# Optimization experiments

Hardware: AMD Instinct MI355X
Metric: run time of the kernel (lower is better)

Reference implementation:

```python
import jax, jax.numpy as jnp
import numpy as np

SPS_AMPLIFY = 1.5
SPS_DAMPEN = 0.3
SPS_DEEP_QUESTION = 0.1
SPS_EXCLAIM = 0.85
SPS_QUESTION = 0.25
SPS_SUPER_EXCLAIM = 0.95

B, S, D = 4, 2048, 1024
NUM_HEADS = 16
HEAD_DIM = D // NUM_HEADS
SCALE = HEAD_DIM ** (-0.5)


def sps_pro(x):
    """Piecewise elementwise modulation based on sigmoid(x) bands."""
    xn = jax.nn.sigmoid(x)
    # bands: xn>0.95 -> 2.0 ; 0.85<xn<=0.95 -> 1.5 ; xn<0.1 -> 0.1 ;
    #        0.1<=xn<0.25 -> 0.3 ; else -> 1.0
    mult = jnp.where(
        xn > SPS_SUPER_EXCLAIM, 2.0,
        jnp.where(xn > SPS_EXCLAIM, SPS_AMPLIFY,
                  jnp.where(xn < SPS_DEEP_QUESTION, 0.1,
                            jnp.where(xn < SPS_QUESTION, SPS_DAMPEN, 1.0))))
    return x * mult


def setup_inputs() -> dict:
    key = jax.random.key(0)
    k0, k1, k2, k3, k4 = jax.random.split(key, 5)
    s = 1.0 / np.sqrt(D)
    return {
        "x": jax.random.normal(k0, (B, S, D), dtype=jnp.float32),
        "W_qkv": jax.random.uniform(k1, (D, 3 * D), dtype=jnp.float32, minval=-s, maxval=s),
        "b_qkv": jax.random.uniform(k2, (3 * D,), dtype=jnp.float32, minval=-s, maxval=s),
        "W_proj": jax.random.uniform(k3, (D, D), dtype=jnp.float32, minval=-s, maxval=s),
        "b_proj": jax.random.uniform(k4, (D,), dtype=jnp.float32, minval=-s, maxval=s),
    }


def reference(x, W_qkv, b_qkv, W_proj, b_proj):
    qkv = jnp.einsum('bsd,de->bse', x, W_qkv) + b_qkv  # [B,S,3D]
    q, k, v = jnp.split(qkv, 3, axis=-1)               # each [B,S,D]
    attn = jnp.einsum('bsd,btd->bst', q, k) * SCALE    # [B,S,S]
    attn = sps_pro(attn)
    attn = jax.nn.softmax(attn, axis=-1)
    out = jnp.einsum('bst,btd->bsd', attn, v)          # [B,S,D]
    out = jnp.einsum('bsd,de->bse', out, W_proj) + b_proj
    return out
```

## Files before the change

### kernel.cpp

```cpp
#include <hip/hip_runtime.h>
#include <hip/hip_bf16.h>
#include <hip/hip_fp16.h>
#include <stdint.h>

typedef __attribute__((ext_vector_type(8))) _Float16 f16x8;
typedef __attribute__((ext_vector_type(4))) float f32x4;

__device__ __forceinline__ void async16(void* lds, const void* g) {
  __builtin_amdgcn_global_load_lds(
      (const __attribute__((address_space(1))) void*)g,
      (__attribute__((address_space(3))) void*)lds, 16, 0, 0);
}

__device__ __forceinline__ uint16_t f2h_u(float f) {
  union { __half h; uint16_t u; } c;
  c.h = __float2half(f);
  return c.u;
}

__global__ __launch_bounds__(256)
void conv_f2h(const float* __restrict__ in, uint16_t* __restrict__ out, int n4) {
  int i = blockIdx.x * 256 + threadIdx.x;
  if (i >= n4) return;
  float4 v = ((const float4*)in)[i];
  ushort4 o;
  o.x = f2h_u(v.x); o.y = f2h_u(v.y); o.z = f2h_u(v.z); o.w = f2h_u(v.w);
  ((ushort4*)out)[i] = o;
}

__global__ __launch_bounds__(256)
void trans_f2h(const float* __restrict__ in, uint16_t* __restrict__ out,
               int ldin, int ldout) {
  __shared__ float t[64][65];
  const int tx = threadIdx.x & 63, ty = threadIdx.x >> 6;
  const int r0 = blockIdx.y * 64, c0 = blockIdx.x * 64;
#pragma unroll
  for (int i = 0; i < 16; ++i)
    t[ty + i * 4][tx] = in[(size_t)(r0 + ty + i * 4) * ldin + c0 + tx];
  __syncthreads();
#pragma unroll
  for (int i = 0; i < 16; ++i)
    out[(size_t)(c0 + ty + i * 4) * ldout + r0 + tx] = f2h_u(t[tx][ty + i * 4]);
}

template <int EPI>
__global__ __launch_bounds__(512, 2)
void gemm8p(const uint16_t* __restrict__ A, const uint16_t* __restrict__ B,
            void* __restrict__ Cv, void* __restrict__ Cv2, void* __restrict__ Cv3,
            const float* __restrict__ bias,
            int nT, int lda, int ldb, int ldc,
            long long strA, long long strB, long long strC) {
  extern __shared__ uint16_t lds_u16[];

  const int gx = gridDim.x, gy = gridDim.y;
  const int nwg = gx * gy * gridDim.z;
  const int fid = blockIdx.x + gx * (blockIdx.y + gy * blockIdx.z);
  const int fs = (fid & 7) * (nwg >> 3) + (fid >> 3);
  const int bx = fs % gx;
  const int by = (fs / gx) % gy;
  const int bz = fs / (gx * gy);

  const int tid = threadIdx.x;
  const int l = tid & 63;
  const int w = tid >> 6;
  const int wm = w >> 2, wn = w & 3;
  const int l15 = l & 15, l4 = l >> 4;
  const int rowBase = bx * 256, colBase = by * 256;
  const uint16_t* Ag = A + (size_t)bz * strA;
  const uint16_t* Bg = B + (size_t)bz * strB;

  const uint16_t* sA[2][2];
  const uint16_t* sB[2][2];
#pragma unroll
  for (int u = 0; u < 2; ++u) {
    int c = tid + (u << 9);
    int cs = c ^ ((c >> 3) & 7);
    int row = cs >> 3, kc = (cs & 7) * 8;
    sA[0][u] = Ag + (size_t)(rowBase + row) * lda + kc;
    sA[1][u] = Ag + (size_t)(rowBase + 128 + row) * lda + kc;
    sB[0][u] = Bg + (size_t)(colBase + row) * ldb + kc;
    sB[1][u] = Bg + (size_t)(colBase + 128 + row) * ldb + kc;
  }

  f32x4 acc[8][4];
#pragma unroll
  for (int m = 0; m < 8; ++m)
#pragma unroll
    for (int n = 0; n < 4; ++n)
      acc[m][n] = (f32x4){0.f, 0.f, 0.f, 0.f};

#define SH_A(buf, h, koff)                                                     \
  {                                                                            \
    const uint32_t d_ = (buf)*32768u + (h)*8192u;                              \
    async16(&lds_u16[d_ + (size_t)tid * 8], sA[h][0] + (koff));                \
    async16(&lds_u16[d_ + (size_t)(tid + 512) * 8], sA[h][1] + (koff));        \
  }
#define SH_B(buf, h, koff)                                                     \
  {                                                                            \
    const uint32_t d_ = (buf)*32768u + 16384u + (h)*8192u;                     \
    async16(&lds_u16[d_ + (size_t)tid * 8], sB[h][0] + (koff));                \
    async16(&lds_u16[d_ + (size_t)(tid + 512) * 8], sB[h][1] + (koff));        \
  }
#define RD_A(dst, buf, mh)                                                     \
  _Pragma("unroll") for (int mr = 0; mr < 4; ++mr) {                           \
    const int lr = (mh)*64 + mr * 16 + l15;                                    \
    const char* hb = (const char*)lds_u16 + (buf)*65536 + wm * 16384;          \
    _Pragma("unroll") for (int ks = 0; ks < 2; ++ks)                           \
      dst[mr][ks] = *(const f16x8*)(hb + lr * 128 +                            \
                    ((ks * 64 + l4 * 16) ^ ((lr & 7) << 4)));                  \
  }
#define RD_B(dst, buf, nh)                                                     \
  _Pragma("unroll") for (int nr = 0; nr < 2; ++nr) {                           \
    const int lr = (wn & 1) * 64 + (nh)*32 + nr * 16 + l15;                    \
    const char* hb = (const char*)lds_u16 + (buf)*65536 + 32768 +              \
                     (wn >> 1) * 16384;                                        \
    _Pragma("unroll") for (int ks = 0; ks < 2; ++ks)                           \
      dst[nr][ks] = *(const f16x8*)(hb + lr * 128 +                            \
                    ((ks * 64 + l4 * 16) ^ ((lr & 7) << 4)));                  \
  }
#define MM(m0, n0, AF, BF)                                                     \
  __builtin_amdgcn_s_setprio(1);                                               \
  _Pragma("unroll") for (int ks = 0; ks < 2; ++ks)                             \
  _Pragma("unroll") for (int mr = 0; mr < 4; ++mr)                             \
  _Pragma("unroll") for (int nr = 0; nr < 2; ++nr)                             \
    acc[(m0) + mr][(n0) + nr] = __builtin_amdgcn_mfma_f32_16x16x32_f16(        \
        AF[mr][ks], BF[nr][ks], acc[(m0) + mr][(n0) + nr], 0, 0, 0);           \
  __builtin_amdgcn_s_setprio(0);
#define VMC(n) asm volatile("s_waitcnt vmcnt(" #n ")" ::: "memory");
#define BAR() __builtin_amdgcn_s_barrier();

  SH_A(0, 0, 0) SH_A(0, 1, 0) SH_B(0, 0, 0) SH_B(0, 1, 0)
  SH_B(1, 0, 64) SH_B(1, 1, 64)
  VMC(4)
  BAR()

  const int nIter = nT >> 1;
  for (int i = 0; i < nIter; ++i) {
    const int e2 = 2 * i + 2, o = 2 * i + 1, o2 = 2 * i + 3;
    const int ke2 = e2 << 6, ko = o << 6, ko2 = o2 << 6;
    f16x8 a0[4][2], a1[4][2], b0[2][2], b1[2][2];
    RD_A(a0, 0, 0) RD_B(b0, 0, 0)
    SH_A(1, 0, ko)
    BAR()
    MM(0, 0, a0, b0)
    RD_B(b1, 0, 1)
    SH_A(1, 1, ko)
    BAR()
    MM(0, 2, a0, b1)
    RD_A(a1, 0, 1)
    if (e2 < nT) SH_B(0, 0, ke2)
    BAR()
    MM(4, 2, a1, b1)
    if (e2 < nT) { SH_B(0, 1, ke2) VMC(4) } else { VMC(0) }
    BAR()
    MM(4, 0, a1, b0)
    RD_A(a0, 1, 0) RD_B(b0, 1, 0)
    if (e2 < nT) SH_A(0, 0, ke2)
    BAR()
    MM(0, 0, a0, b0)
    RD_B(b1, 1, 1)
    if (e2 < nT) SH_A(0, 1, ke2)
    BAR()
    MM(0, 2, a0, b1)
    RD_A(a1, 1, 1)
    if (o2 < nT) SH_B(1, 0, ko2)
    BAR()
    MM(4, 2, a1, b1)
    if (o2 < nT) { SH_B(1, 1, ko2) }
    if (i + 1 < nIter) { if (o2 < nT) { VMC(4) } else { VMC(0) } }
    BAR()
    MM(4, 0, a1, b0)
  }
#undef SH_A
#undef SH_B
#undef RD_A
#undef RD_B
#undef MM
#undef VMC
#undef BAR

  if (EPI == 0) {
    uint16_t* qd = (uint16_t*)Cv;
    uint16_t* kd = (uint16_t*)Cv2;
    uint16_t* vt = (uint16_t*)Cv3;
#pragma unroll
    for (int ni = 0; ni < 4; ++ni) {
      const int gcol = colBase + wn * 64 + ni * 16 + l15;
      const float bv = bias[gcol];
      if (gcol < 2048) {
        uint16_t* base = (gcol < 1024 ? qd : kd) + (gcol & 1023);
#pragma unroll
        for (int mi = 0; mi < 8; ++mi)
#pragma unroll
          for (int j = 0; j < 4; ++j) {
            const int grow = rowBase + wm * 128 + mi * 16 + l4 * 4 + j;
            base[(size_t)(grow >> 11) * 2097152 + (size_t)(grow & 2047) * 1024] =
                f2h_u(acc[mi][ni][j] + bv);
          }
      } else {
        const int d = gcol - 2048;
#pragma unroll
        for (int mi = 0; mi < 8; ++mi) {
          const int grow0 = rowBase + wm * 128 + mi * 16 + l4 * 4;
          ushort4 o;
          o.x = f2h_u(acc[mi][ni][0] + bv);
          o.y = f2h_u(acc[mi][ni][1] + bv);
          o.z = f2h_u(acc[mi][ni][2] + bv);
          o.w = f2h_u(acc[mi][ni][3] + bv);
          *(ushort4*)&vt[(size_t)(grow0 >> 11) * 2097152 + (size_t)d * 2048 +
                         (grow0 & 2047)] = o;
        }
      }
    }
  } else {
    uint16_t* C = (uint16_t*)Cv + (size_t)bz * strC;
#pragma unroll
    for (int ni = 0; ni < 4; ++ni) {
      const int gcol = colBase + wn * 64 + ni * 16 + l15;
#pragma unroll
      for (int mi = 0; mi < 8; ++mi)
#pragma unroll
        for (int j = 0; j < 4; ++j) {
          const int grow = rowBase + wm * 128 + mi * 16 + l4 * 4 + j;
          float xs = acc[mi][ni][j] * 0.125f;
          float mult = (xs > 2.94443897916644f) ? 2.0f
                     : (xs > 1.73460105538811f) ? 1.5f
                     : (xs < -2.19722457733622f) ? 0.1f
                     : (xs < -1.09861228866811f) ? 0.3f
                                                 : 1.0f;
          C[(size_t)grow * ldc + gcol] = f2h_u(xs * mult);
        }
    }
  }
}

template <int EPI>
__global__ __launch_bounds__(512, 2)
void gemm_sm(const uint16_t* __restrict__ A, const uint16_t* __restrict__ B,
             void* __restrict__ Cv, const float* __restrict__ bias,
             int nT, int lda, int ldb, int ldc,
             long long strA, long long strB, long long strC) {
  extern __shared__ uint16_t lds_u16[];

  const int gx = gridDim.x, gy = gridDim.y;
  const int nwg = gx * gy * gridDim.z;
  const int fid = blockIdx.x + gx * (blockIdx.y + gy * blockIdx.z);
  const int fs = (fid & 7) * (nwg >> 3) + (fid >> 3);
  const int bx = fs % gx;
  const int by = (fs / gx) % gy;
  const int bz = fs / (gx * gy);

  const int tid = threadIdx.x;
  const int l = tid & 63;
  const int w = tid >> 6;
  const int wm = w >> 1, wn = w & 1;
  const int l15 = l & 15, l4 = l >> 4;
  const int rowBase = bx * 256, colBase = by * 128;
  const uint16_t* Ag = A + (size_t)bz * strA;
  const uint16_t* Bg = B + (size_t)bz * strB;

  const uint16_t* pA[4];
  const uint16_t* pB[2];
#pragma unroll
  for (int u = 0; u < 4; ++u) {
    int c = tid + (u << 9);
    int cs = c ^ ((c >> 3) & 7);
    pA[u] = Ag + (size_t)(rowBase + (cs >> 3)) * lda + (cs & 7) * 8;
  }
#pragma unroll
  for (int u = 0; u < 2; ++u) {
    int c = tid + (u << 9);
    int cs = c ^ ((c >> 3) & 7);
    pB[u] = Bg + (size_t)(colBase + (cs >> 3)) * ldb + (cs & 7) * 8;
  }

  f32x4 acc[4][4];
#pragma unroll
  for (int m = 0; m < 4; ++m)
#pragma unroll
    for (int n = 0; n < 4; ++n)
      acc[m][n] = (f32x4){0.f, 0.f, 0.f, 0.f};

#define STAGE(t2, s2)                                                          \
  {                                                                            \
    const int kb_ = (t2) << 6;                                                 \
    uint16_t* dA_ = lds_u16 + (s2) * 24576;                                    \
    uint16_t* dB_ = dA_ + 16384;                                               \
    _Pragma("unroll") for (int u = 0; u < 4; ++u)                              \
        async16(&dA_[(size_t)(tid + (u << 9)) * 8], pA[u] + kb_);              \
    _Pragma("unroll") for (int u = 0; u < 2; ++u)                              \
        async16(&dB_[(size_t)(tid + (u << 9)) * 8], pB[u] + kb_);              \
  }

  STAGE(0, 0)
  STAGE(1, 1)
  asm volatile("s_waitcnt vmcnt(6)" ::: "memory");
  __builtin_amdgcn_s_barrier();

  int sl = 0;
  for (int t = 0; t < nT; ++t) {
    int s2 = sl + 2; if (s2 >= 3) s2 -= 3;
    if (t + 2 < nT) STAGE(t + 2, s2)
    const uint16_t* As = lds_u16 + sl * 24576;
    const uint16_t* Bs = As + 16384;
#pragma unroll
    for (int ks = 0; ks < 2; ++ks) {
      f16x8 af[4], bf[4];
#pragma unroll
      for (int m = 0; m < 4; ++m) {
        const int r = wm * 64 + m * 16 + l15;
        const int byt = r * 128 + ((ks * 64 + l4 * 16) ^ ((r & 7) << 4));
        af[m] = *(const f16x8*)((const char*)As + byt);
      }
#pragma unroll
      for (int n = 0; n < 4; ++n) {
        const int r = wn * 64 + n * 16 + l15;
        const int byt = r * 128 + ((ks * 64 + l4 * 16) ^ ((r & 7) << 4));
        bf[n] = *(const f16x8*)((const char*)Bs + byt);
      }
      __builtin_amdgcn_s_setprio(1);
#pragma unroll
      for (int m = 0; m < 4; ++m)
#pragma unroll
        for (int n = 0; n < 4; ++n)
          acc[m][n] = __builtin_amdgcn_mfma_f32_16x16x32_f16(af[m], bf[n], acc[m][n], 0, 0, 0);
      __builtin_amdgcn_s_setprio(0);
    }
    if (t + 1 < nT) {
      if (t + 2 < nT) {
        asm volatile("s_waitcnt vmcnt(6)" ::: "memory");
      } else {
        asm volatile("s_waitcnt vmcnt(0)" ::: "memory");
      }
      __builtin_amdgcn_s_barrier();
    }
    sl = (sl == 2) ? 0 : sl + 1;
  }
#undef STAGE

  const int orow0 = rowBase + wm * 64 + l4 * 4;
  const int ocol0 = colBase + wn * 64 + l15;
  if (EPI == 3) {
    uint16_t* C = (uint16_t*)Cv + (size_t)bz * strC;
#pragma unroll
    for (int n = 0; n < 4; ++n)
#pragma unroll
      for (int m = 0; m < 4; ++m)
#pragma unroll
        for (int j = 0; j < 4; ++j)
          C[(size_t)(orow0 + m * 16 + j) * ldc + ocol0 + n * 16] = f2h_u(acc[m][n][j]);
  } else {
    float* C = (float*)Cv;
#pragma unroll
    for (int n = 0; n < 4; ++n) {
      const float bv = bias[ocol0 + n * 16];
#pragma unroll
      for (int m = 0; m < 4; ++m)
#pragma unroll
        for (int j = 0; j < 4; ++j)
          C[(size_t)(orow0 + m * 16 + j) * ldc + ocol0 + n * 16] = acc[m][n][j] + bv;
    }
  }
}

__global__ __launch_bounds__(256)
void softmax_rows(uint16_t* __restrict__ P) {
  const size_t row = blockIdx.x;
  uint16_t* p = P + row * 2048;
  const int tid = threadIdx.x;
  uint4 raw = *(const uint4*)(p + tid * 8);
  uint32_t w[4] = {raw.x, raw.y, raw.z, raw.w};
  float v[8];
#pragma unroll
  for (int q = 0; q < 4; ++q) {
    __half2 h = *(__half2*)&w[q];
    float2 f = __half22float2(h);
    v[2 * q] = f.x;
    v[2 * q + 1] = f.y;
  }
  float mx = v[0];
#pragma unroll
  for (int j = 1; j < 8; ++j) mx = fmaxf(mx, v[j]);
#pragma unroll
  for (int o = 32; o > 0; o >>= 1) mx = fmaxf(mx, __shfl_xor(mx, o));
  __shared__ float redm[4], reds[4];
  if ((tid & 63) == 0) redm[tid >> 6] = mx;
  __syncthreads();
  mx = fmaxf(fmaxf(redm[0], redm[1]), fmaxf(redm[2], redm[3]));
  float e[8];
  float se = 0.f;
#pragma unroll
  for (int j = 0; j < 8; ++j) { e[j] = __expf(v[j] - mx); se += e[j]; }
#pragma unroll
  for (int o = 32; o > 0; o >>= 1) se += __shfl_xor(se, o);
  if ((tid & 63) == 0) reds[tid >> 6] = se;
  __syncthreads();
  se = (reds[0] + reds[1]) + (reds[2] + reds[3]);
  const float inv = 1.0f / se;
  uint32_t wo[4];
#pragma unroll
  for (int q = 0; q < 4; ++q) {
    uint16_t a = f2h_u(e[2 * q] * inv);
    uint16_t b = f2h_u(e[2 * q + 1] * inv);
    wo[q] = (uint32_t)a | ((uint32_t)b << 16);
  }
  uint4 ov;
  ov.x = wo[0]; ov.y = wo[1]; ov.z = wo[2]; ov.w = wo[3];
  *(uint4*)(p + tid * 8) = ov;
}

extern "C" void kernel_launch(void* const* d_in, const int* in_sizes, int n_in,
                              void* d_out, int out_size, void* d_ws, size_t ws_size,
                              hipStream_t stream) {
  const float* x     = (const float*)d_in[0];
  const float* Wqkv  = (const float*)d_in[1];
  const float* bqkv  = (const float*)d_in[2];
  const float* Wproj = (const float*)d_in[3];
  const float* bproj = (const float*)d_in[4];
  float* out = (float*)d_out;

  char* ws = (char*)d_ws;
  size_t off = 0;
  auto alloc = [&](size_t bytes) -> void* {
    void* p = ws + off;
    off += (bytes + 255) & ~(size_t)255;
    return p;
  };
  uint16_t* xh    = (uint16_t*)alloc(8192ULL * 1024 * 2);
  uint16_t* WqkvT = (uint16_t*)alloc(3072ULL * 1024 * 2);
  uint16_t* WpT   = (uint16_t*)alloc(1024ULL * 1024 * 2);
  uint16_t* qh    = (uint16_t*)alloc(4ULL * 2048 * 1024 * 2);
  uint16_t* kh    = (uint16_t*)alloc(4ULL * 2048 * 1024 * 2);
  uint16_t* vT    = (uint16_t*)alloc(4ULL * 1024 * 2048 * 2);
  uint16_t* Pm    = (uint16_t*)alloc(4ULL * 2048 * 2048 * 2);
  uint16_t* ao    = xh;

  conv_f2h<<<8192, 256, 0, stream>>>(x, xh, 2097152);
  trans_f2h<<<dim3(48, 16), 256, 0, stream>>>(Wqkv, WqkvT, 3072, 1024);
  trans_f2h<<<dim3(16, 16), 256, 0, stream>>>(Wproj, WpT, 1024, 1024);
  gemm8p<0><<<dim3(32, 12, 1), 512, 131072, stream>>>(
      xh, WqkvT, qh, kh, vT, bqkv, 16, 1024, 1024, 0, 0, 0, 0);
  gemm8p<1><<<dim3(8, 8, 4), 512, 131072, stream>>>(
      qh, kh, Pm, nullptr, nullptr, nullptr, 16, 1024, 1024, 2048,
      2097152LL, 2097152LL, 4194304LL);
  softmax_rows<<<8192, 256, 0, stream>>>(Pm);
  gemm_sm<3><<<dim3(8, 8, 4), 512, 147456, stream>>>(
      Pm, vT, ao, nullptr, 32, 2048, 2048, 1024,
      4194304LL, 2097152LL, 2097152LL);
  gemm_sm<4><<<dim3(32, 8, 1), 512, 147456, stream>>>(
      ao, WpT, out, bproj, 16, 1024, 1024, 1024, 0, 0, 0);
}
```

Baseline: 214.7 us.

## Use smaller 128x128 double-buffered GEMM tiles for attention and projection

Replaces the 256x128 triple-buffered 512-thread GEMM with a 128x128 tile, 256-thread, double-buffered variant using 64KB LDS. The QK^T GEMM moves from the large gemm8p kernel onto this new kernel, with the sps modulation epilogue folded into it. The intent is more workgroups, lower LDS use and better occupancy and wave balance across CUs. The cost is less data reuse per tile and a shallower prefetch pipeline, since each step now waits for vmcnt(0).

Measured after the change: 214.8 us. Within noise of the previous version (+0.0%).

```diff
diff --git a/kernel.cpp b/kernel.cpp
--- a/kernel.cpp
+++ b/kernel.cpp
@@ -212,31 +212,12 @@
         }
       }
     }
-  } else {
-    uint16_t* C = (uint16_t*)Cv + (size_t)bz * strC;
-#pragma unroll
-    for (int ni = 0; ni < 4; ++ni) {
-      const int gcol = colBase + wn * 64 + ni * 16 + l15;
-#pragma unroll
-      for (int mi = 0; mi < 8; ++mi)
-#pragma unroll
-        for (int j = 0; j < 4; ++j) {
-          const int grow = rowBase + wm * 128 + mi * 16 + l4 * 4 + j;
-          float xs = acc[mi][ni][j] * 0.125f;
-          float mult = (xs > 2.94443897916644f) ? 2.0f
-                     : (xs > 1.73460105538811f) ? 1.5f
-                     : (xs < -2.19722457733622f) ? 0.1f
-                     : (xs < -1.09861228866811f) ? 0.3f
-                                                 : 1.0f;
-          C[(size_t)grow * ldc + gcol] = f2h_u(xs * mult);
-        }
-    }
   }
 }
 
 template <int EPI>
-__global__ __launch_bounds__(512, 2)
-void gemm_sm(const uint16_t* __restrict__ A, const uint16_t* __restrict__ B,
+__global__ __launch_bounds__(256, 2)
+void gemm_mb(const uint16_t* __restrict__ A, const uint16_t* __restrict__ B,
              void* __restrict__ Cv, const float* __restrict__ bias,
              int nT, int lda, int ldb, int ldc,
              long long strA, long long strB, long long strC) {
@@ -255,22 +236,17 @@
   const int w = tid >> 6;
   const int wm = w >> 1, wn = w & 1;
   const int l15 = l & 15, l4 = l >> 4;
-  const int rowBase = bx * 256, colBase = by * 128;
+  const int rowBase = bx * 128, colBase = by * 128;
   const uint16_t* Ag = A + (size_t)bz * strA;
   const uint16_t* Bg = B + (size_t)bz * strB;
 
   const uint16_t* pA[4];
-  const uint16_t* pB[2];
+  const uint16_t* pB[4];
 #pragma unroll
   for (int u = 0; u < 4; ++u) {
-    int c = tid + (u << 9);
+    int c = tid + (u << 8);
     int cs = c ^ ((c >> 3) & 7);
     pA[u] = Ag + (size_t)(rowBase + (cs >> 3)) * lda + (cs & 7) * 8;
-  }
-#pragma unroll
-  for (int u = 0; u < 2; ++u) {
-    int c = tid + (u << 9);
-    int cs = c ^ ((c >> 3) & 7);
     pB[u] = Bg + (size_t)(colBase + (cs >> 3)) * ldb + (cs & 7) * 8;
   }
 
@@ -284,25 +260,23 @@
 #define STAGE(t2, s2)                                                          \
   {                                                                            \
     const int kb_ = (t2) << 6;                                                 \
-    uint16_t* dA_ = lds_u16 + (s2) * 24576;                                    \
-    uint16_t* dB_ = dA_ + 16384;                                               \
-    _Pragma("unroll") for (int u = 0; u < 4; ++u)                              \
-        async16(&dA_[(size_t)(tid + (u << 9)) * 8], pA[u] + kb_);              \
-    _Pragma("unroll") for (int u = 0; u < 2; ++u)                              \
-        async16(&dB_[(size_t)(tid + (u << 9)) * 8], pB[u] + kb_);              \
+    uint16_t* dA_ = lds_u16 + (s2)*16384;                                      \
+    uint16_t* dB_ = dA_ + 8192;                                                \
+    _Pragma("unroll") for (int u = 0; u < 4; ++u) {                            \
+      async16(&dA_[(size_t)(tid + (u << 8)) * 8], pA[u] + kb_);                \
+      async16(&dB_[(size_t)(tid + (u << 8)) * 8], pB[u] + kb_);                \
+    }                                                                          \
   }
 
   STAGE(0, 0)
-  STAGE(1, 1)
-  asm volatile("s_waitcnt vmcnt(6)" ::: "memory");
+  asm volatile("s_waitcnt vmcnt(0)" ::: "memory");
   __builtin_amdgcn_s_barrier();
 
-  int sl = 0;
   for (int t = 0; t < nT; ++t) {
-    int s2 = sl + 2; if (s2 >= 3) s2 -= 3;
-    if (t + 2 < nT) STAGE(t + 2, s2)
-    const uint16_t* As = lds_u16 + sl * 24576;
-    const uint16_t* Bs = As + 16384;
+    const int s = t & 1;
+    if (t + 1 < nT) STAGE(t + 1, s ^ 1)
+    const uint16_t* As = lds_u16 + s * 16384;
+    const uint16_t* Bs = As + 8192;
 #pragma unroll
     for (int ks = 0; ks < 2; ++ks) {
       f16x8 af[4], bf[4];
@@ -327,20 +301,31 @@
       __builtin_amdgcn_s_setprio(0);
     }
     if (t + 1 < nT) {
-      if (t + 2 < nT) {
-        asm volatile("s_waitcnt vmcnt(6)" ::: "memory");
-      } else {
-        asm volatile("s_waitcnt vmcnt(0)" ::: "memory");
-      }
+      asm volatile("s_waitcnt vmcnt(0)" ::: "memory");
       __builtin_amdgcn_s_barrier();
     }
-    sl = (sl == 2) ? 0 : sl + 1;
   }
 #undef STAGE
 
   const int orow0 = rowBase + wm * 64 + l4 * 4;
   const int ocol0 = colBase + wn * 64 + l15;
-  if (EPI == 3) {
+  if (EPI == 1) {
+    uint16_t* C = (uint16_t*)Cv + (size_t)bz * strC;
+#pragma unroll
+    for (int n = 0; n < 4; ++n)
+#pragma unroll
+      for (int m = 0; m < 4; ++m)
+#pragma unroll
+        for (int j = 0; j < 4; ++j) {
+          float xs = acc[m][n][j] * 0.125f;
+          float mult = (xs > 2.94443897916644f) ? 2.0f
+                     : (xs > 1.73460105538811f) ? 1.5f
+                     : (xs < -2.19722457733622f) ? 0.1f
+                     : (xs < -1.09861228866811f) ? 0.3f
+                                                 : 1.0f;
+          C[(size_t)(orow0 + m * 16 + j) * ldc + ocol0 + n * 16] = f2h_u(xs * mult);
+        }
+  } else if (EPI == 3) {
     uint16_t* C = (uint16_t*)Cv + (size_t)bz * strC;
 #pragma unroll
     for (int n = 0; n < 4; ++n)
@@ -440,13 +425,13 @@
   trans_f2h<<<dim3(16, 16), 256, 0, stream>>>(Wproj, WpT, 1024, 1024);
   gemm8p<0><<<dim3(32, 12, 1), 512, 131072, stream>>>(
       xh, WqkvT, qh, kh, vT, bqkv, 16, 1024, 1024, 0, 0, 0, 0);
-  gemm8p<1><<<dim3(8, 8, 4), 512, 131072, stream>>>(
-      qh, kh, Pm, nullptr, nullptr, nullptr, 16, 1024, 1024, 2048,
+  gemm_mb<1><<<dim3(16, 16, 4), 256, 65536, stream>>>(
+      qh, kh, Pm, nullptr, 16, 1024, 1024, 2048,
       2097152LL, 2097152LL, 4194304LL);
   softmax_rows<<<8192, 256, 0, stream>>>(Pm);
-  gemm_sm<3><<<dim3(8, 8, 4), 512, 147456, stream>>>(
+  gemm_mb<3><<<dim3(16, 8, 4), 256, 65536, stream>>>(
       Pm, vT, ao, nullptr, 32, 2048, 2048, 1024,
       4194304LL, 2097152LL, 2097152LL);
-  gemm_sm<4><<<dim3(32, 8, 1), 512, 147456, stream>>>(
+  gemm_mb<4><<<dim3(64, 8, 1), 256, 65536, stream>>>(
       ao, WpT, out, bproj, 16, 1024, 1024, 1024, 0, 0, 0);
 }
```
